# Kernel tuning notes

Hardware: AMD Instinct MI355X
Metric: run time of the kernel (lower is better)

Reference implementation:

```python
import jax, jax.numpy as jnp
import numpy as np

B = 262144
L = 16      # latent_dim
H = 64      # hidden_dim
C = 8       # num_charts
O = 32      # output_dim
TAU_MIN = 0.01
TAU_DENOM_MIN = 0.001
EPS = 0.001
LN_EPS = 1e-5


def setup_inputs() -> dict:
    key = jax.random.key(0)
    ks = jax.random.split(key, 16)
    # latents kept well inside the Poincare ball
    z_geo = 0.1 * jax.random.normal(ks[0], (B, L), dtype=jnp.float32)
    z_tex = 0.1 * jax.random.normal(ks[1], (B, L), dtype=jnp.float32)
    def lin(k, fan_in, shape):
        bound = 1.0 / np.sqrt(fan_in)
        return jax.random.uniform(k, shape, jnp.float32, -bound, bound)
    chart_w = lin(ks[2], L, (C, H, L))   # stacked per-chart Linear weights
    chart_b = lin(ks[3], L, (C, H))
    router_w = lin(ks[4], L, (C, L))
    router_b = lin(ks[5], L, (C,))
    centers = 0.02 * jax.random.normal(ks[6], (C, L), dtype=jnp.float32)
    tex_w = lin(ks[7], L, (H, L))
    tex_b = lin(ks[8], L, (H,))
    ln_g = jnp.ones((H,), jnp.float32)
    ln_b = jnp.zeros((H,), jnp.float32)
    w1 = lin(ks[9], H, (H, H))
    b1 = lin(ks[10], H, (H,))
    w2 = lin(ks[11], H, (O, H))
    b2 = lin(ks[12], H, (O,))
    return dict(z_geo=z_geo, z_tex=z_tex, chart_w=chart_w, chart_b=chart_b,
                router_w=router_w, router_b=router_b, centers=centers,
                tex_w=tex_w, tex_b=tex_b, ln_g=ln_g, ln_b=ln_b,
                w1=w1, b1=b1, w2=w2, b2=b2)


def _temperature(z):
    r2 = jnp.sum(z * z, axis=-1)                      # [B]
    denom = jnp.maximum(1.0 - r2, TAU_DENOM_MIN)
    tau = (np.sqrt(L) * denom) * 0.5
    return jnp.maximum(tau, TAU_MIN)                  # [B]


def _gelu(x):
    return jax.nn.gelu(x, approximate=False)


def reference(z_geo, z_tex, chart_w, chart_b, router_w, router_b, centers,
              tex_w, tex_b, ln_g, ln_b, w1, b1, w2, b2):
    # hyperbolic distance scores  [B, C]
    diff = z_geo[:, None, :] - centers[None, :, :]
    dist_sq = jnp.sum(diff * diff, axis=-1)
    z_sq = jnp.sum(z_geo * z_geo, axis=-1, keepdims=True)   # [B,1]
    c_sq = jnp.sum(centers * centers, axis=-1)[None, :]      # [1,C]
    denom = (1.0 - z_sq) * (1.0 - c_sq)
    arg = 1.0 + 2.0 * dist_sq / (denom + EPS)
    dist = jnp.arccosh(jnp.maximum(arg, 1.0 + EPS))
    tau = _temperature(z_geo)                                # [B]
    scores = -dist / tau[:, None]
    scores = scores + 0.1 * (z_geo @ router_w.T + router_b) / tau[:, None]
    router_weights = jax.nn.softmax(scores, axis=-1)         # [B,C]

    # dense chart projection + weighted blend
    h_stack = jnp.einsum('bl,chl->bch', z_geo, chart_w) + chart_b[None]  # [B,C,H]
    h_global = jnp.sum(h_stack * router_weights[:, :, None], axis=1)     # [B,H]
    h_tex = z_tex @ tex_w.T + tex_b
    h = h_global + h_tex

    # renderer: LayerNorm -> GELU -> Linear -> GELU -> Linear
    mu = jnp.mean(h, axis=-1, keepdims=True)
    var = jnp.mean((h - mu) ** 2, axis=-1, keepdims=True)
    hn = (h - mu) * jax.lax.rsqrt(var + LN_EPS) * ln_g + ln_b
    h1 = _gelu(_gelu(hn) @ w1.T + b1)
    x_hat = h1 @ w2.T + b2
    return x_hat, router_weights
```

## Files before the change

kernel.cpp:

```cpp
#include <hip/hip_runtime.h>
#include <hip/hip_bf16.h>
#include <hip/hip_fp16.h>


typedef __attribute__((ext_vector_type(8))) short short8;
typedef __attribute__((ext_vector_type(4))) float f32x4;

__device__ __forceinline__ int pkbf2(float a, float b) {
    union { __hip_bfloat162 h2; int i; } u;
    u.h2 = __float22bfloat162_rn(make_float2(a, b));
    return u.i;
}
__device__ __forceinline__ short pkbf1(float a) { return (short)pkbf2(a, 0.f); }

__device__ __forceinline__ float gelu_fast(float x) {
    float x2 = x * x;
    float t  = __expf(fmaf(x2, 0.07135481f, 1.5957691f) * x);
    float r  = __builtin_amdgcn_rcpf(t + 1.0f);
    return fmaf(-x, r, x);
}
__device__ __forceinline__ int bpack(int k, int n, int KT) {
    return (((n >> 4) * KT + (k >> 5)) * 64 + (n & 15) + (((k & 31) >> 3) << 4)) * 8 + (k & 7);
}
__device__ __forceinline__ int gswz(int g) {
    return g ^ (((g >> 4) & 3) << 1) ^ ((g >> 3) & 1);
}
__device__ __forceinline__ short8 packrow8(const float* base) {
    const float4* p = (const float4*)base;
    float4 a = p[0], b = p[1];
    union { short8 s; int i[4]; } f;
    f.i[0] = pkbf2(a.x, a.y); f.i[1] = pkbf2(a.z, a.w);
    f.i[2] = pkbf2(b.x, b.y); f.i[3] = pkbf2(b.z, b.w);
    return f.s;
}

__global__ void pack_weights(const float* __restrict__ cw, const float* __restrict__ cb,
                             const float* __restrict__ txw, const float* __restrict__ txb,
                             const float* __restrict__ w1,  const float* __restrict__ w2,
                             const float* __restrict__ cen, const float* __restrict__ rb,
                             short* __restrict__ ws)
{
    const int tid = threadIdx.x;
    const int b = blockIdx.x;
    if (b < 40) {
        int idx = b * 256 + tid;
        int k = idx >> 6, n = idx & 63;
        float v;
        if (k < 128)       v = cw[(k >> 4) * 1024 + n * 16 + (k & 15)];
        else if (k < 144)  v = txw[n * 16 + (k - 128)];
        else if (k < 152)  v = cb[(k - 144) * 64 + n];
        else if (k == 152) v = txb[n];
        else               v = 0.f;
        ws[bpack(k, n, 5)] = pkbf1(v);
    } else if (b == 40) {
        for (int f = tid; f < 512; f += 256) {
            int lane = f & 63, e = f >> 6;
            int nt = e >> 1, kt = e & 1;
            int col = lane & 15, qq = lane >> 4;
            *(short8*)(ws + 10240 + f * 8) =
                packrow8(w1 + (nt * 16 + col) * 64 + kt * 32 + qq * 8);
        }
    } else if (b == 41) {
        int f = tid;
        int lane = f & 63, e = f >> 6;
        int nt = e >> 1, kt = e & 1;
        int col = lane & 15, qq = lane >> 4;
        *(short8*)(ws + 14336 + f * 8) =
            packrow8(w2 + (nt * 16 + col) * 64 + kt * 32 + qq * 8);
    } else {
        if (tid < 8) {
            float csq = 0.f;
            for (int l = 0; l < 16; l++) { float cv = cen[tid * 16 + l]; csq = fmaf(cv, cv, csq); }
            ((float4*)((char*)ws + 32768))[tid] =
                make_float4(csq, 1.0f - csq, 0.1f * rb[tid], 0.f);
        }
    }
}

constexpr int SCR_OFF = 20480;
constexpr int W2L_OFF = 28672;
constexpr int SMEM_SZ = 32768;

__global__ __launch_bounds__(256, 5) void topo_mfma(
    const float* __restrict__ zg,  const float* __restrict__ ztx,
    const float* __restrict__ cw,  const float* __restrict__ cb,
    const float* __restrict__ rw,  const float* __restrict__ rb,
    const float* __restrict__ cen, const float* __restrict__ txw,
    const float* __restrict__ txb, const float* __restrict__ lng,
    const float* __restrict__ lnb, const float* __restrict__ w1,
    const float* __restrict__ b1,  const float* __restrict__ w2,
    const float* __restrict__ b2,  const short* __restrict__ wsp,
    const int prepacked,
    float* __restrict__ out, int Btot)
{
    __shared__ __align__(16) char smem[SMEM_SZ];
    short* WA = (short*)smem;
    const short8* W2L = (const short8*)(smem + W2L_OFF);

    const int tid = threadIdx.x;
    const int wv = tid >> 6, lane = tid & 63;
    const int q = lane >> 4, col = lane & 15;
    const int sub = (lane >> 3) & 1, j = lane & 7;

    if (prepacked) {
        const int4* src = (const int4*)wsp;
        int4* dst = (int4*)smem;
        #pragma unroll
        for (int i = 0; i < 5; i++) dst[i * 256 + tid] = src[i * 256 + tid];
        ((int4*)(smem + W2L_OFF))[tid] = ((const int4*)((const char*)wsp + 28672))[tid];
    } else {
        for (int idx = tid; idx < 160 * 64; idx += 256) {
            int k = idx >> 6, n = idx & 63;
            float v;
            if (k < 128)       v = cw[(k >> 4) * 1024 + n * 16 + (k & 15)];
            else if (k < 144)  v = txw[n * 16 + (k - 128)];
            else if (k < 152)  v = cb[(k - 144) * 64 + n];
            else if (k == 152) v = txb[n];
            else               v = 0.f;
            WA[bpack(k, n, 5)] = pkbf1(v);
        }
        {
            int e = tid >> 6, ln = tid & 63;
            int nt = e >> 1, kt = e & 1;
            *(short8*)(smem + W2L_OFF + (e * 64 + ln) * 16) =
                packrow8(w2 + (nt * 16 + (ln & 15)) * 64 + kt * 32 + (ln >> 4) * 8);
        }
    }

    const long sG = (long)blockIdx.x * 256 + tid;
    int4 rsh;
    {
        float z[16];
        const float4* pg = (const float4*)(zg + sG * 16);
        #pragma unroll
        for (int v = 0; v < 4; v++) {
            float4 a = pg[v];
            z[v*4+0]=a.x; z[v*4+1]=a.y; z[v*4+2]=a.z; z[v*4+3]=a.w;
        }
        float r2 = 0.f;
        #pragma unroll
        for (int l = 0; l < 16; l++) r2 = fmaf(z[l], z[l], r2);
        const float inv_tau = __builtin_amdgcn_rcpf(fmaxf(2.0f * fmaxf(1.0f - r2, 0.001f), 0.01f));
        const float omr2 = 1.0f - r2;
        const float4* cvp = (const float4*)((const char*)wsp + 32768);
        float scv[8]; float smax = -1e30f;
        #pragma unroll
        for (int c = 0; c < 8; c++) {
            float csq, omc2, rb1;
            if (prepacked) {
                float4 kv = cvp[c]; csq = kv.x; omc2 = kv.y; rb1 = kv.z;
            } else {
                csq = 0.f;
                #pragma unroll
                for (int l = 0; l < 16; l++) { float cv = cen[c*16+l]; csq = fmaf(cv, cv, csq); }
                omc2 = 1.0f - csq; rb1 = 0.1f * rb[c];
            }
            const float4* cp = (const float4*)(cen + c * 16);
            const float4* rp = (const float4*)(rw  + c * 16);
            float zc = 0.f, dotv = 0.f;
            #pragma unroll
            for (int v = 0; v < 4; v++) {
                float4 cv = cp[v], rv = rp[v];
                zc   = fmaf(z[v*4+0],cv.x, fmaf(z[v*4+1],cv.y,
                       fmaf(z[v*4+2],cv.z, fmaf(z[v*4+3],cv.w, zc))));
                dotv = fmaf(z[v*4+0],rv.x, fmaf(z[v*4+1],rv.y,
                       fmaf(z[v*4+2],rv.z, fmaf(z[v*4+3],rv.w, dotv))));
            }
            float dsq = fmaf(-2.0f, zc, r2 + csq);
            float u = 2.0f * dsq * __builtin_amdgcn_rcpf(omr2 * omc2 + 0.001f);
            u = fmaxf(u, 0.001f);
            float dist  = __logf((1.0f + u) + __builtin_amdgcn_sqrtf(u * (u + 2.0f)));
            float score = (fmaf(0.1f, dotv, rb1) - dist) * inv_tau;
            scv[c] = score; smax = fmaxf(smax, score);
        }
        float esum = 0.f;
        #pragma unroll
        for (int c = 0; c < 8; c++) { scv[c] = __expf(scv[c] - smax); esum += scv[c]; }
        const float rinv = __builtin_amdgcn_rcpf(esum);
        union { ushort us[8]; int4 v; } hv;
        #pragma unroll
        for (int c = 0; c < 8; c++) {
            scv[c] *= rinv;
            hv.us[(c & 1) * 4 + (c >> 1)] = __half_as_ushort(__float2half_rn(scv[c]));
        }
        rsh = hv.v;
        float4* pr = (float4*)(out + (long)Btot * 32 + sG * 8);
        pr[0] = make_float4(scv[0], scv[1], scv[2], scv[3]);
        pr[1] = make_float4(scv[4], scv[5], scv[6], scv[7]);
    }

    short8 W1F[4][2];
    if (prepacked) {
        const short8* p1 = (const short8*)(wsp + 10240);
        #pragma unroll
        for (int nt = 0; nt < 4; nt++)
            #pragma unroll
            for (int kt = 0; kt < 2; kt++)
                W1F[nt][kt] = p1[(nt * 2 + kt) * 64 + lane];
    } else {
        const int kb = q * 8;
        #pragma unroll
        for (int nt = 0; nt < 4; nt++)
            #pragma unroll
            for (int kt = 0; kt < 2; kt++)
                W1F[nt][kt] = packrow8(w1 + (nt * 16 + col) * 64 + kt * 32 + kb);
    }
    float lngv[4], lnbv[4], b1v[4], b2v[2];
    #pragma unroll
    for (int nt = 0; nt < 4; nt++) {
        lngv[nt] = lng[nt * 16 + col];
        lnbv[nt] = lnb[nt * 16 + col];
        b1v[nt]  = b1[nt * 16 + col];
    }
    b2v[0] = b2[col]; b2v[1] = b2[16 + col];

    __syncthreads();

    short* scr = (short*)(smem + SCR_OFF) + wv * 1024;
    union Frag { short8 s; int i[4]; };

    const long blockBase = (long)blockIdx.x * 256;
    const float* zrow = zg  + (blockBase + wv * 64 + col) * 16 + ((q & 1) << 3);
    const float* trow = ztx + (blockBase + wv * 64 + col) * 16 + ((q & 1) << 3);

    float4 za = ((const float4*)zrow)[0], zb = ((const float4*)zrow)[1];
    float4 ta = ((const float4*)trow)[0], tb = ((const float4*)trow)[1];

    for (int t = 0; t < 4; t++) {
        const int  mBase = wv * 64 + t * 16;
        const int  srcLn = t * 16 + col;

        int4 got;
        got.x = __shfl(rsh.x, srcLn);
        got.y = __shfl(rsh.y, srcLn);
        got.z = __shfl(rsh.z, srcLn);
        got.w = __shfl(rsh.w, srcLn);

        float rc[4];
        {
            int w0 = (q < 2) ? got.x : got.z;
            int w1s = (q < 2) ? got.y : got.w;
            float2 f0 = __half22float2(*(__half2*)&w0);
            float2 f1 = __half22float2(*(__half2*)&w1s);
            rc[0] = f0.x; rc[1] = f0.y; rc[2] = f1.x; rc[3] = f1.y;
        }

        f32x4 acc[4] = {{0.f,0.f,0.f,0.f},{0.f,0.f,0.f,0.f},{0.f,0.f,0.f,0.f},{0.f,0.f,0.f,0.f}};
        #pragma unroll
        for (int kt = 0; kt < 4; kt++) {
            float r = rc[kt];
            Frag f;
            f.i[0] = pkbf2(r * za.x, r * za.y);
            f.i[1] = pkbf2(r * za.z, r * za.w);
            f.i[2] = pkbf2(r * zb.x, r * zb.y);
            f.i[3] = pkbf2(r * zb.z, r * zb.w);
            #pragma unroll
            for (int nt = 0; nt < 4; nt++) {
                short8 bf = *(const short8*)(WA + (nt * 5 + kt) * 512 + lane * 8);
                acc[nt] = __builtin_amdgcn_mfma_f32_16x16x32_bf16(f.s, bf, acc[nt], 0, 0, 0);
            }
        }
        {
            Frag f;
            if (q < 2) {
                f.i[0] = pkbf2(ta.x, ta.y); f.i[1] = pkbf2(ta.z, ta.w);
                f.i[2] = pkbf2(tb.x, tb.y); f.i[3] = pkbf2(tb.z, tb.w);
            } else if (q == 2) {
                float2 e0 = __half22float2(*(__half2*)&got.x);
                float2 e1 = __half22float2(*(__half2*)&got.y);
                float2 e2 = __half22float2(*(__half2*)&got.z);
                float2 e3 = __half22float2(*(__half2*)&got.w);
                f.i[0] = pkbf2(e0.x, e2.x);
                f.i[1] = pkbf2(e0.y, e2.y);
                f.i[2] = pkbf2(e1.x, e3.x);
                f.i[3] = pkbf2(e1.y, e3.y);
            } else {
                f.i[0] = pkbf2(1.0f, 0.f); f.i[1] = 0; f.i[2] = 0; f.i[3] = 0;
            }
            #pragma unroll
            for (int nt = 0; nt < 4; nt++) {
                short8 bf = *(const short8*)(WA + (nt * 5 + 4) * 512 + lane * 8);
                acc[nt] = __builtin_amdgcn_mfma_f32_16x16x32_bf16(f.s, bf, acc[nt], 0, 0, 0);
            }
        }

        if (t < 3) {
            const float4* pzn = (const float4*)(zrow + (t + 1) * 256);
            const float4* ptn = (const float4*)(trow + (t + 1) * 256);
            za = pzn[0]; zb = pzn[1]; ta = ptn[0]; tb = ptn[1];
        }

        float mu[4], rsd[4];
        #pragma unroll
        for (int reg = 0; reg < 4; reg++) {
            float a = acc[0][reg], b = acc[1][reg], c = acc[2][reg], d = acc[3][reg];
            float s  = (a + b) + (c + d);
            float s2 = fmaf(a, a, fmaf(b, b, fmaf(c, c, d * d)));
            s  += __shfl_xor(s, 1);  s  += __shfl_xor(s, 2);
            s  += __shfl_xor(s, 4);  s  += __shfl_xor(s, 8);
            s2 += __shfl_xor(s2, 1); s2 += __shfl_xor(s2, 2);
            s2 += __shfl_xor(s2, 4); s2 += __shfl_xor(s2, 8);
            float m = s * (1.0f / 64.0f);
            mu[reg]  = m;
            rsd[reg] = rsqrtf(fmaf(s2, 1.0f / 64.0f, -m * m) + 1e-5f);
        }

        #pragma unroll
        for (int nt = 0; nt < 4; nt++) {
            int high = (nt & 1) * 2 + sub;
            #pragma unroll
            for (int reg = 0; reg < 4; reg++) {
                float hn = (acc[nt][reg] - mu[reg]) * rsd[reg] * lngv[nt] + lnbv[nt];
                int grp = gswz((q * 4 + reg) + 16 * high);
                scr[(nt >> 1) * 512 + grp * 8 + j] = pkbf1(gelu_fast(hn));
            }
        }
        asm volatile("s_waitcnt lgkmcnt(0)" ::: "memory");

        short8 A2[2];
        {
            int grp = gswz(lane);
            A2[0] = *(const short8*)(scr +       grp * 8);
            A2[1] = *(const short8*)(scr + 512 + grp * 8);
        }

        #pragma unroll
        for (int nt = 0; nt < 4; nt++) {
            f32x4 a2 = {0.f, 0.f, 0.f, 0.f};
            a2 = __builtin_amdgcn_mfma_f32_16x16x32_bf16(A2[0], W1F[nt][0], a2, 0, 0, 0);
            a2 = __builtin_amdgcn_mfma_f32_16x16x32_bf16(A2[1], W1F[nt][1], a2, 0, 0, 0);
            int high = (nt & 1) * 2 + sub;
            #pragma unroll
            for (int reg = 0; reg < 4; reg++) {
                float h1v = gelu_fast(a2[reg] + b1v[nt]);
                int grp = gswz((q * 4 + reg) + 16 * high);
                scr[(nt >> 1) * 512 + grp * 8 + j] = pkbf1(h1v);
            }
        }
        asm volatile("s_waitcnt lgkmcnt(0)" ::: "memory");

        short8 A3[2];
        {
            int grp = gswz(lane);
            A3[0] = *(const short8*)(scr +       grp * 8);
            A3[1] = *(const short8*)(scr + 512 + grp * 8);
        }

        const long sOutBase = blockBase + mBase + q * 4;
        #pragma unroll
        for (int nt = 0; nt < 2; nt++) {
            f32x4 a3 = {0.f, 0.f, 0.f, 0.f};
            short8 wA = W2L[(nt * 2 + 0) * 64 + lane];
            short8 wB = W2L[(nt * 2 + 1) * 64 + lane];
            a3 = __builtin_amdgcn_mfma_f32_16x16x32_bf16(A3[0], wA, a3, 0, 0, 0);
            a3 = __builtin_amdgcn_mfma_f32_16x16x32_bf16(A3[1], wB, a3, 0, 0, 0);
            #pragma unroll
            for (int reg = 0; reg < 4; reg++)
                out[(sOutBase + reg) * 32 + nt * 16 + col] = a3[reg] + b2v[nt];
        }
    }
}

extern "C" void kernel_launch(void* const* d_in, const int* in_sizes, int n_in,
                              void* d_out, int out_size, void* d_ws, size_t ws_size,
                              hipStream_t stream) {
    const int B = in_sizes[0] / 16;
    const int prepacked = (d_ws != nullptr && ws_size >= 32896) ? 1 : 0;
    if (prepacked) {
        hipLaunchKernelGGL(pack_weights, dim3(43), dim3(256), 0, stream,
            (const float*)d_in[2],  (const float*)d_in[3],
            (const float*)d_in[7],  (const float*)d_in[8],
            (const float*)d_in[11], (const float*)d_in[13],
            (const float*)d_in[6],  (const float*)d_in[5],
            (short*)d_ws);
    }
    dim3 grid(B / 256), block(256);
    hipLaunchKernelGGL(topo_mfma, grid, block, 0, stream,
        (const float*)d_in[0],  (const float*)d_in[1],
        (const float*)d_in[2],  (const float*)d_in[3],
        (const float*)d_in[4],  (const float*)d_in[5],
        (const float*)d_in[6],  (const float*)d_in[7],
        (const float*)d_in[8],  (const float*)d_in[9],
        (const float*)d_in[10], (const float*)d_in[11],
        (const float*)d_in[12], (const float*)d_in[13],
        (const float*)d_in[14],
        (const short*)d_ws, prepacked,
        (float*)d_out, B);
}
```

Measured before the change: 162.0 us.

## Swap second-layer MFMA operands and pass activations via lane shuffles instead of LDS

The W1 layer MFMA now puts the weights in the A operand, producing a transposed output tile. Packed bf16 results are redistributed across lanes with xor-32/xor-16 shuffles to form the A fragment of the final layer, removing an LDS write/wait/read round-trip. Because of the transposed layout, b1 is read from LDS as a float4 per lane rather than held in registers. Launch bounds drop from 5 to 4 blocks per CU, which may lower occupancy in exchange for more registers.

```diff
diff --git a/kernel.cpp b/kernel.cpp
--- a/kernel.cpp
+++ b/kernel.cpp
@@ -34,10 +34,34 @@
     return f.s;
 }
 
+__device__ __forceinline__ void bfly(int (&D)[4][2], bool hi32, bool hi16) {
+    #pragma unroll
+    for (int n1 = 0; n1 < 2; n1++)
+        #pragma unroll
+        for (int s = 0; s < 2; s++) {
+            int d0 = D[n1*2+0][s], d1 = D[n1*2+1][s];
+            int send = hi32 ? d0 : d1;
+            int recv = __shfl_xor(send, 32);
+            D[n1*2+0][s] = hi32 ? recv : d0;
+            D[n1*2+1][s] = hi32 ? d1 : recv;
+        }
+    #pragma unroll
+    for (int n1 = 0; n1 < 2; n1++)
+        #pragma unroll
+        for (int s = 0; s < 2; s++) {
+            int d0 = D[n1*2+0][s], d1 = D[n1*2+1][s];
+            int send = hi16 ? d0 : d1;
+            int recv = __shfl_xor(send, 16);
+            D[n1*2+0][s] = hi16 ? recv : d0;
+            D[n1*2+1][s] = hi16 ? d1 : recv;
+        }
+}
+
 __global__ void pack_weights(const float* __restrict__ cw, const float* __restrict__ cb,
                              const float* __restrict__ txw, const float* __restrict__ txb,
                              const float* __restrict__ w1,  const float* __restrict__ w2,
                              const float* __restrict__ cen, const float* __restrict__ rb,
+                             const float* __restrict__ b1,
                              short* __restrict__ ws)
 {
     const int tid = threadIdx.x;
@@ -74,14 +98,16 @@
             ((float4*)((char*)ws + 32768))[tid] =
                 make_float4(csq, 1.0f - csq, 0.1f * rb[tid], 0.f);
         }
+        if (tid < 64) ((float*)((char*)ws + 32896))[tid] = b1[tid];
     }
 }
 
 constexpr int SCR_OFF = 20480;
 constexpr int W2L_OFF = 28672;
-constexpr int SMEM_SZ = 32768;
-
-__global__ __launch_bounds__(256, 5) void topo_mfma(
+constexpr int B1L_OFF = 32768;
+constexpr int SMEM_SZ = 33024;
+
+__global__ __launch_bounds__(256, 4) void topo_mfma(
     const float* __restrict__ zg,  const float* __restrict__ ztx,
     const float* __restrict__ cw,  const float* __restrict__ cb,
     const float* __restrict__ rw,  const float* __restrict__ rb,
@@ -96,11 +122,13 @@
     __shared__ __align__(16) char smem[SMEM_SZ];
     short* WA = (short*)smem;
     const short8* W2L = (const short8*)(smem + W2L_OFF);
+    const float* B1L = (const float*)(smem + B1L_OFF);
 
     const int tid = threadIdx.x;
     const int wv = tid >> 6, lane = tid & 63;
     const int q = lane >> 4, col = lane & 15;
     const int sub = (lane >> 3) & 1, j = lane & 7;
+    const bool hi32 = (lane & 32) != 0, hi16 = (lane & 16) != 0;
 
     if (prepacked) {
         const int4* src = (const int4*)wsp;
@@ -108,6 +136,8 @@
         #pragma unroll
         for (int i = 0; i < 5; i++) dst[i * 256 + tid] = src[i * 256 + tid];
         ((int4*)(smem + W2L_OFF))[tid] = ((const int4*)((const char*)wsp + 28672))[tid];
+        if (tid < 16)
+            ((int4*)(smem + B1L_OFF))[tid] = ((const int4*)((const char*)wsp + 32896))[tid];
     } else {
         for (int idx = tid; idx < 160 * 64; idx += 256) {
             int k = idx >> 6, n = idx & 63;
@@ -125,6 +155,7 @@
             *(short8*)(smem + W2L_OFF + (e * 64 + ln) * 16) =
                 packrow8(w2 + (nt * 16 + (ln & 15)) * 64 + kt * 32 + (ln >> 4) * 8);
         }
+        if (tid < 64) ((float*)(smem + B1L_OFF))[tid] = b1[tid];
     }
 
     const long sG = (long)blockIdx.x * 256 + tid;
@@ -205,12 +236,11 @@
             for (int kt = 0; kt < 2; kt++)
                 W1F[nt][kt] = packrow8(w1 + (nt * 16 + col) * 64 + kt * 32 + kb);
     }
-    float lngv[4], lnbv[4], b1v[4], b2v[2];
+    float lngv[4], lnbv[4], b2v[2];
     #pragma unroll
     for (int nt = 0; nt < 4; nt++) {
         lngv[nt] = lng[nt * 16 + col];
         lnbv[nt] = lnb[nt * 16 + col];
-        b1v[nt]  = b1[nt * 16 + col];
     }
     b2v[0] = b2[col]; b2v[1] = b2[16 + col];
 
@@ -324,27 +354,24 @@
             A2[1] = *(const short8*)(scr + 512 + grp * 8);
         }
 
+        int D2[4][2];
         #pragma unroll
         for (int nt = 0; nt < 4; nt++) {
             f32x4 a2 = {0.f, 0.f, 0.f, 0.f};
-            a2 = __builtin_amdgcn_mfma_f32_16x16x32_bf16(A2[0], W1F[nt][0], a2, 0, 0, 0);
-            a2 = __builtin_amdgcn_mfma_f32_16x16x32_bf16(A2[1], W1F[nt][1], a2, 0, 0, 0);
-            int high = (nt & 1) * 2 + sub;
-            #pragma unroll
-            for (int reg = 0; reg < 4; reg++) {
-                float h1v = gelu_fast(a2[reg] + b1v[nt]);
-                int grp = gswz((q * 4 + reg) + 16 * high);
-                scr[(nt >> 1) * 512 + grp * 8 + j] = pkbf1(h1v);
-            }
-        }
-        asm volatile("s_waitcnt lgkmcnt(0)" ::: "memory");
-
-        short8 A3[2];
-        {
-            int grp = gswz(lane);
-            A3[0] = *(const short8*)(scr +       grp * 8);
-            A3[1] = *(const short8*)(scr + 512 + grp * 8);
-        }
+            a2 = __builtin_amdgcn_mfma_f32_16x16x32_bf16(W1F[nt][0], A2[0], a2, 0, 0, 0);
+            a2 = __builtin_amdgcn_mfma_f32_16x16x32_bf16(W1F[nt][1], A2[1], a2, 0, 0, 0);
+            float4 o4 = *(const float4*)(B1L + nt * 16 + q * 4);
+            float h0 = gelu_fast(a2[0] + o4.x);
+            float h1 = gelu_fast(a2[1] + o4.y);
+            float h2 = gelu_fast(a2[2] + o4.z);
+            float h3 = gelu_fast(a2[3] + o4.w);
+            D2[nt][0] = pkbf2(h0, h1);
+            D2[nt][1] = pkbf2(h2, h3);
+        }
+        bfly(D2, hi32, hi16);
+        Frag A3f0, A3f1;
+        A3f0.i[0]=D2[0][0]; A3f0.i[1]=D2[0][1]; A3f0.i[2]=D2[1][0]; A3f0.i[3]=D2[1][1];
+        A3f1.i[0]=D2[2][0]; A3f1.i[1]=D2[2][1]; A3f1.i[2]=D2[3][0]; A3f1.i[3]=D2[3][1];
 
         const long sOutBase = blockBase + mBase + q * 4;
         #pragma unroll
@@ -352,8 +379,8 @@
             f32x4 a3 = {0.f, 0.f, 0.f, 0.f};
             short8 wA = W2L[(nt * 2 + 0) * 64 + lane];
             short8 wB = W2L[(nt * 2 + 1) * 64 + lane];
-            a3 = __builtin_amdgcn_mfma_f32_16x16x32_bf16(A3[0], wA, a3, 0, 0, 0);
-            a3 = __builtin_amdgcn_mfma_f32_16x16x32_bf16(A3[1], wB, a3, 0, 0, 0);
+            a3 = __builtin_amdgcn_mfma_f32_16x16x32_bf16(A3f0.s, wA, a3, 0, 0, 0);
+            a3 = __builtin_amdgcn_mfma_f32_16x16x32_bf16(A3f1.s, wB, a3, 0, 0, 0);
             #pragma unroll
             for (int reg = 0; reg < 4; reg++)
                 out[(sOutBase + reg) * 32 + nt * 16 + col] = a3[reg] + b2v[nt];
@@ -365,13 +392,14 @@
                               void* d_out, int out_size, void* d_ws, size_t ws_size,
                               hipStream_t stream) {
     const int B = in_sizes[0] / 16;
-    const int prepacked = (d_ws != nullptr && ws_size >= 32896) ? 1 : 0;
+    const int prepacked = (d_ws != nullptr && ws_size >= 33152) ? 1 : 0;
     if (prepacked) {
         hipLaunchKernelGGL(pack_weights, dim3(43), dim3(256), 0, stream,
             (const float*)d_in[2],  (const float*)d_in[3],
             (const float*)d_in[7],  (const float*)d_in[8],
             (const float*)d_in[11], (const float*)d_in[13],
             (const float*)d_in[6],  (const float*)d_in[5],
+            (const float*)d_in[12],
             (short*)d_ws);
     }
     dim3 grid(B / 256), block(256);
```

Result: faster. 141.2 us (-12.8%).

## Software-pipeline stage-1 of next tile with MLP stages using double scratch

Applied to the files above, without the earlier changes.

Splits the per-tile LDS scratch into two buffers so the router/chart/LayerNorm stage for the next tile runs between the W1 GEMM and the W2 GEMM of the current tile. The aim is to interleave independent MFMA and ALU work and hide LDS write-read latency behind it. In exchange, shared memory per block grows and launch bounds drop from 5 to 4 blocks per CU, which lowers occupancy and likely raises register pressure.

```diff
diff --git a/kernel.cpp b/kernel.cpp
--- a/kernel.cpp
+++ b/kernel.cpp
@@ -77,11 +77,12 @@
     }
 }
 
-constexpr int SCR_OFF = 20480;
-constexpr int W2L_OFF = 28672;
-constexpr int SMEM_SZ = 32768;
-
-__global__ __launch_bounds__(256, 5) void topo_mfma(
+constexpr int SCRA_OFF = 20480;
+constexpr int SCRB_OFF = 28672;
+constexpr int W2L_OFF  = 36864;
+constexpr int SMEM_SZ  = 40960;
+
+__global__ __launch_bounds__(256, 4) void topo_mfma(
     const float* __restrict__ zg,  const float* __restrict__ ztx,
     const float* __restrict__ cw,  const float* __restrict__ cb,
     const float* __restrict__ rw,  const float* __restrict__ rb,
@@ -216,7 +217,8 @@
 
     __syncthreads();
 
-    short* scr = (short*)(smem + SCR_OFF) + wv * 1024;
+    short* scrA = (short*)(smem + SCRA_OFF) + wv * 1024;
+    short* scrB = (short*)(smem + SCRB_OFF) + wv * 1024;
     union Frag { short8 s; int i[4]; };
 
     const long blockBase = (long)blockIdx.x * 256;
@@ -226,16 +228,13 @@
     float4 za = ((const float4*)zrow)[0], zb = ((const float4*)zrow)[1];
     float4 ta = ((const float4*)trow)[0], tb = ((const float4*)trow)[1];
 
-    for (int t = 0; t < 4; t++) {
-        const int  mBase = wv * 64 + t * 16;
-        const int  srcLn = t * 16 + col;
-
+    auto ADVANCE = [&](int tn) {
+        const int srcLn = tn * 16 + col;
         int4 got;
         got.x = __shfl(rsh.x, srcLn);
         got.y = __shfl(rsh.y, srcLn);
         got.z = __shfl(rsh.z, srcLn);
         got.w = __shfl(rsh.w, srcLn);
-
         float rc[4];
         {
             int w0 = (q < 2) ? got.x : got.z;
@@ -284,9 +283,9 @@
             }
         }
 
-        if (t < 3) {
-            const float4* pzn = (const float4*)(zrow + (t + 1) * 256);
-            const float4* ptn = (const float4*)(trow + (t + 1) * 256);
+        if (tn < 3) {
+            const float4* pzn = (const float4*)(zrow + (tn + 1) * 256);
+            const float4* ptn = (const float4*)(trow + (tn + 1) * 256);
             za = pzn[0]; zb = pzn[1]; ta = ptn[0]; tb = ptn[1];
         }
 
@@ -312,41 +311,52 @@
             for (int reg = 0; reg < 4; reg++) {
                 float hn = (acc[nt][reg] - mu[reg]) * rsd[reg] * lngv[nt] + lnbv[nt];
                 int grp = gswz((q * 4 + reg) + 16 * high);
-                scr[(nt >> 1) * 512 + grp * 8 + j] = pkbf1(gelu_fast(hn));
-            }
-        }
-        asm volatile("s_waitcnt lgkmcnt(0)" ::: "memory");
-
-        short8 A2[2];
-        {
-            int grp = gswz(lane);
-            A2[0] = *(const short8*)(scr +       grp * 8);
-            A2[1] = *(const short8*)(scr + 512 + grp * 8);
-        }
-
+                scrA[(nt >> 1) * 512 + grp * 8 + j] = pkbf1(gelu_fast(hn));
+            }
+        }
+    };
+
+    short8 A2cur[2];
+    ADVANCE(0);
+    asm volatile("s_waitcnt lgkmcnt(0)" ::: "memory");
+    {
+        int grp = gswz(lane);
+        A2cur[0] = *(const short8*)(scrA +       grp * 8);
+        A2cur[1] = *(const short8*)(scrA + 512 + grp * 8);
+    }
+
+    for (int t = 0; t < 4; t++) {
         #pragma unroll
         for (int nt = 0; nt < 4; nt++) {
             f32x4 a2 = {0.f, 0.f, 0.f, 0.f};
-            a2 = __builtin_amdgcn_mfma_f32_16x16x32_bf16(A2[0], W1F[nt][0], a2, 0, 0, 0);
-            a2 = __builtin_amdgcn_mfma_f32_16x16x32_bf16(A2[1], W1F[nt][1], a2, 0, 0, 0);
+            a2 = __builtin_amdgcn_mfma_f32_16x16x32_bf16(A2cur[0], W1F[nt][0], a2, 0, 0, 0);
+            a2 = __builtin_amdgcn_mfma_f32_16x16x32_bf16(A2cur[1], W1F[nt][1], a2, 0, 0, 0);
             int high = (nt & 1) * 2 + sub;
             #pragma unroll
             for (int reg = 0; reg < 4; reg++) {
                 float h1v = gelu_fast(a2[reg] + b1v[nt]);
                 int grp = gswz((q * 4 + reg) + 16 * high);
-                scr[(nt >> 1) * 512 + grp * 8 + j] = pkbf1(h1v);
-            }
-        }
+                scrB[(nt >> 1) * 512 + grp * 8 + j] = pkbf1(h1v);
+            }
+        }
+
+        if (t < 3) ADVANCE(t + 1);
+
         asm volatile("s_waitcnt lgkmcnt(0)" ::: "memory");
 
         short8 A3[2];
         {
             int grp = gswz(lane);
-            A3[0] = *(const short8*)(scr +       grp * 8);
-            A3[1] = *(const short8*)(scr + 512 + grp * 8);
-        }
-
-        const long sOutBase = blockBase + mBase + q * 4;
+            A3[0] = *(const short8*)(scrB +       grp * 8);
+            A3[1] = *(const short8*)(scrB + 512 + grp * 8);
+        }
+        if (t < 3) {
+            int grp = gswz(lane);
+            A2cur[0] = *(const short8*)(scrA +       grp * 8);
+            A2cur[1] = *(const short8*)(scrA + 512 + grp * 8);
+        }
+
+        const long sOutBase = blockBase + wv * 64 + t * 16 + q * 4;
         #pragma unroll
         for (int nt = 0; nt < 2; nt++) {
             f32x4 a3 = {0.f, 0.f, 0.f, 0.f};
```

New measurement: 143.8 us. -11.2%, faster.
